# Optimization experiments

Measured on AMD Instinct MI355X. Metric: run time of the kernel, lower is better.

The kernel has to match this reference:

```python
import jax, jax.numpy as jnp
import numpy as np

N_NODES = 110
C = 4096  # in_channels = hidden = out_channels


def setup_inputs() -> dict:
    key = jax.random.key(0)
    ks = jax.random.split(key, 8)
    x = jax.random.normal(ks[0], (N_NODES, C), dtype=jnp.float32)
    adj = jax.random.randint(ks[1], (N_NODES, N_NODES), 0, 2, dtype=jnp.int32)
    # torch.nn.Linear weights stored [out_features, in_features]
    W2 = jax.random.normal(ks[2], (C, C), dtype=jnp.float32) / np.sqrt(C)
    b2 = jax.random.normal(ks[3], (C,), dtype=jnp.float32) * 0.01
    W1 = jax.random.normal(ks[4], (2 * C, C), dtype=jnp.float32) / np.sqrt(2 * C)
    b1 = jax.random.normal(ks[5], (C,), dtype=jnp.float32) * 0.01
    Wl = jax.random.normal(ks[6], (N_NODES, N_NODES), dtype=jnp.float32) / np.sqrt(N_NODES)
    bl = jax.random.normal(ks[7], (N_NODES,), dtype=jnp.float32) * 0.01
    # note: W1 is stored [in=2C, out=C]; W2 [in=C, out=C]; Wl [in=110, out=110]
    return {"x": x, "adj": adj, "W2": W2, "b2": b2, "W1": W1, "b1": b1, "Wl": Wl, "bl": bl}


def reference(x, adj, W2, b2, W1, b1, Wl, bl):
    # FeatGraphConv: h = lin2(x)
    h = x @ W2 + b2  # [N, C]
    # edge_index.nonzero(): adjacency -> edge list (i=src, j=dst); mean-aggregate
    # h[src] at dst. Dense equivalent: column-normalized mask matmul.
    mask = (adj != 0).astype(x.dtype)  # [N, N]
    deg = mask.sum(axis=0)  # in-degree of each target node j
    aggr = (mask.T @ h) / jnp.maximum(deg, 1.0)[:, None]  # [N, C]; 0 for isolated nodes (PyG mean)
    # update: lin1(cat(h, aggr)) then relu (in RegGNN.forward)
    out = jax.nn.relu(jnp.concatenate([h, aggr], axis=1) @ W1 + b1)  # [N, C]
    # x.t(); lin(110,110); x.t()
    out = (out.T @ Wl.T + bl).T  # [N, C]
    return out
```

## Files before the change

kernel.cpp:

```cpp
#include <hip/hip_runtime.h>
#include <hip/hip_fp16.h>

#define C 4096
#define NN 110
#define MPAD 112
#define BN 256
#define BK 32
#define ASTR 40

typedef _Float16 f16x8 __attribute__((ext_vector_type(8)));
typedef _Float16 f16x4 __attribute__((ext_vector_type(4)));
typedef float fx4 __attribute__((ext_vector_type(4)));

#define AS_GLB __attribute__((address_space(1)))
#define AS_LDS __attribute__((address_space(3)))

__global__ void prep1_kernel(const float* __restrict__ x, _Float16* __restrict__ A1) {
    int idx = blockIdx.x * 256 + threadIdx.x;
    int n = idx >> 12;
    float v = (n < NN) ? x[idx] : 0.f;
    A1[idx] = (_Float16)v;
}

__global__ __launch_bounds__(256, 2)
void mm_kernel(const _Float16* __restrict__ A, const float* __restrict__ B,
               float* __restrict__ Cacc, int lda, int kch) {
    __shared__ float    Bs[BK * BN];
    __shared__ _Float16 As[MPAD * ASTR];

    const int t   = threadIdx.x;
    const int w   = t >> 6;
    const int L   = t & 63;
    const int l15 = L & 15;
    const int q   = L >> 4;
    const int n0  = blockIdx.x * BN;
    const int k0  = blockIdx.y * kch;

    fx4 acc[7][4];
    #pragma unroll
    for (int mt = 0; mt < 7; ++mt)
        #pragma unroll
        for (int nt = 0; nt < 4; ++nt)
            acc[mt][nt] = (fx4){0.f, 0.f, 0.f, 0.f};

    #pragma unroll 1
    for (int kc = 0; kc < kch; kc += BK) {
        #pragma unroll
        for (int j = 0; j < 8; ++j) {
            const int row = w * 8 + j;
            const float* g = B + (size_t)(k0 + kc + row) * C + n0 + L * 4;
            __builtin_amdgcn_global_load_lds((const AS_GLB void*)g,
                                             (AS_LDS void*)(Bs + row * BN), 16, 0, 0);
        }
        #pragma unroll
        for (int i = 0; i < 4; ++i) {
            int idx = t + i * 256;
            if (idx < MPAD * 8) {
                int row = idx >> 3;
                int c4  = (idx & 7) * 4;
                f16x4 v = *(const f16x4*)(A + (size_t)row * lda + k0 + kc + c4);
                *(f16x4*)(As + row * ASTR + c4) = v;
            }
        }
        __syncthreads();
        f16x8 bfrag[4];
        #pragma unroll
        for (int nt = 0; nt < 4; ++nt)
            #pragma unroll
            for (int j = 0; j < 8; ++j)
                bfrag[nt][j] = (_Float16)Bs[(q * 8 + j) * BN + w * 64 + nt * 16 + l15];
        #pragma unroll
        for (int mt = 0; mt < 7; ++mt) {
            f16x8 af = *(const f16x8*)(As + (mt * 16 + l15) * ASTR + q * 8);
            #pragma unroll
            for (int nt = 0; nt < 4; ++nt)
                acc[mt][nt] = __builtin_amdgcn_mfma_f32_16x16x32_f16(af, bfrag[nt],
                                                                     acc[mt][nt], 0, 0, 0);
        }
        __syncthreads();
    }

    #pragma unroll
    for (int mt = 0; mt < 7; ++mt) {
        #pragma unroll
        for (int nt = 0; nt < 4; ++nt) {
            const int col = n0 + w * 64 + nt * 16 + l15;
            #pragma unroll
            for (int r = 0; r < 4; ++r) {
                int row = mt * 16 + q * 4 + r;
                if (row < NN)
                    atomicAdd(&Cacc[(size_t)row * C + col], acc[mt][nt][r]);
            }
        }
    }
}

__global__ __launch_bounds__(256)
void agg_kernel(const float* __restrict__ h_raw, const int* __restrict__ adj,
                const float* __restrict__ b2, _Float16* __restrict__ A3) {
    __shared__ float hb[NN * 16];
    __shared__ unsigned long long mlo[NN], mhi[NN];
    __shared__ float degs[NN];
    const int t  = threadIdx.x;
    const int c0 = blockIdx.x * 16;

    for (int idx = t; idx < NN * 16; idx += 256) {
        int n = idx >> 4, c = idx & 15;
        float v = h_raw[(size_t)n * C + c0 + c] + b2[c0 + c];
        hb[idx] = v;
        A3[(size_t)n * (2 * C) + c0 + c] = (_Float16)v;
    }
    if (t < 64) {
        int n  = NN + (t >> 5);
        int hs = (t >> 4) & 1;
        int c  = t & 15;
        A3[(size_t)n * (2 * C) + hs * C + c0 + c] = (_Float16)0.f;
    }
    if (t < NN) {
        int j = t;
        unsigned long long lo = 0, hi = 0;
        int dg = 0;
        for (int i = 0; i < 64; ++i) {
            int m = (adj[i * NN + j] != 0);
            lo |= ((unsigned long long)m) << i; dg += m;
        }
        for (int i = 64; i < NN; ++i) {
            int m = (adj[i * NN + j] != 0);
            hi |= ((unsigned long long)m) << (i - 64); dg += m;
        }
        mlo[j] = lo; mhi[j] = hi;
        degs[j] = (float)(dg > 0 ? dg : 1);
    }
    __syncthreads();
    for (int idx = t; idx < NN * 16; idx += 256) {
        int j = idx >> 4, c = idx & 15;
        unsigned long long lo = mlo[j], hi = mhi[j];
        float a = 0.f;
        #pragma unroll 2
        for (int i = 0; i < 64; ++i)
            a = fmaf((float)((lo >> i) & 1ull), hb[i * 16 + c], a);
        #pragma unroll 2
        for (int i = 64; i < NN; ++i)
            a = fmaf((float)((hi >> (i - 64)) & 1ull), hb[i * 16 + c], a);
        A3[(size_t)j * (2 * C) + C + c0 + c] = (_Float16)(a / degs[j]);
    }
}

__global__ __launch_bounds__(256)
void fin_kernel(const float* __restrict__ z_raw, const float* __restrict__ b1,
                const float* __restrict__ Wl, const float* __restrict__ bl,
                float* __restrict__ out) {
    __shared__ float zs[NN * 64];
    const int t  = threadIdx.x;
    const int c0 = blockIdx.x * 64;
    const int j  = blockIdx.y * 4 + (t >> 6);
    const int c  = t & 63;

    for (int idx = t; idx < NN * 64; idx += 256) {
        int k = idx >> 6, cc = idx & 63;
        float v = z_raw[(size_t)k * C + c0 + cc] + b1[c0 + cc];
        zs[idx] = fmaxf(v, 0.f);
    }
    __syncthreads();
    if (j < NN) {
        float a = bl[j];
        #pragma unroll 2
        for (int k = 0; k < NN; ++k)
            a += Wl[j * NN + k] * zs[k * 64 + c];
        out[(size_t)j * C + c0 + c] = a;
    }
}

extern "C" void kernel_launch(void* const* d_in, const int* in_sizes, int n_in,
                              void* d_out, int out_size, void* d_ws, size_t ws_size,
                              hipStream_t stream) {
    const float* x   = (const float*)d_in[0];
    const int*   adj = (const int*)d_in[1];
    const float* W2  = (const float*)d_in[2];
    const float* b2  = (const float*)d_in[3];
    const float* W1  = (const float*)d_in[4];
    const float* b1  = (const float*)d_in[5];
    const float* Wl  = (const float*)d_in[6];
    const float* bl  = (const float*)d_in[7];
    float* out = (float*)d_out;

    char* ws = (char*)d_ws;
    float*    h_raw = (float*)(ws);
    float*    z_raw = (float*)(ws + 1802240);
    _Float16* A1    = (_Float16*)(ws + 3604480);
    _Float16* A3    = (_Float16*)(ws + 4521984);

    hipMemsetAsync(d_ws, 0, 3604480, stream);
    prep1_kernel<<<(MPAD * C) / 256, 256, 0, stream>>>(x, A1);
    mm_kernel<<<dim3(C / BN, 32), 256, 0, stream>>>(A1, W2, h_raw, C, 128);
    agg_kernel<<<C / 16, 256, 0, stream>>>(h_raw, adj, b2, A3);
    mm_kernel<<<dim3(C / BN, 32), 256, 0, stream>>>(A3, W1, z_raw, 2 * C, 256);
    fin_kernel<<<dim3(C / 64, 28), 256, 0, stream>>>(z_raw, b1, Wl, bl, out);
}
```

Baseline: 414.9 us.

## Repack weights to tiled fp16, double-buffer GEMM, replace atomics with split-K partial sums

Adds a repack kernel that converts the fp32 weights into fp16 tiles laid out for MFMA B fragments, so the GEMM loads them directly with no per-element conversion in LDS. The GEMM now double-buffers its LDS stages, uses narrower 128-column tiles, and writes split-K partials to a buffer instead of issuing atomicAdds. Separate reductions in agg and a new zred kernel sum those partials. The repack runs on every call, which adds extra weight read and write traffic.

```diff
diff --git a/kernel.cpp b/kernel.cpp
--- a/kernel.cpp
+++ b/kernel.cpp
@@ -4,9 +4,6 @@
 #define C 4096
 #define NN 110
 #define MPAD 112
-#define BN 256
-#define BK 32
-#define ASTR 40
 
 typedef _Float16 f16x8 __attribute__((ext_vector_type(8)));
 typedef _Float16 f16x4 __attribute__((ext_vector_type(4)));
@@ -14,6 +11,43 @@
 
 #define AS_GLB __attribute__((address_space(1)))
 #define AS_LDS __attribute__((address_space(3)))
+
+__global__ __launch_bounds__(256, 2)
+void repack_kernel(const float* __restrict__ W, _Float16* __restrict__ B16, int K) {
+    __shared__ _Float16 Ls[1024 * 36];
+    const int t  = threadIdx.x;
+    const int kt = blockIdx.x;
+    const int cs = blockIdx.y;
+    const int Kt = K >> 5;
+
+    const float* src = W + (size_t)(kt * 32) * C + cs * 1024;
+    #pragma unroll 4
+    for (int i = 0; i < 32; ++i) {
+        int idx = t + i * 256;
+        int r   = idx >> 8;
+        int c4  = (idx & 255) * 4;
+        fx4 v = *(const fx4*)(src + (size_t)r * C + c4);
+        #pragma unroll
+        for (int j = 0; j < 4; ++j)
+            Ls[(c4 + j) * 36 + r] = (_Float16)v[j];
+    }
+    __syncthreads();
+    #pragma unroll 4
+    for (int i = 0; i < 16; ++i) {
+        int o   = t + i * 256;
+        int kk8 = (o & 3) * 8;
+        int c   = (o >> 2) & 127;
+        int nt8 = o >> 9;
+        const _Float16* lp = Ls + (nt8 * 128 + c) * 36 + kk8;
+        f16x4 a = *(const f16x4*)(lp);
+        f16x4 b = *(const f16x4*)(lp + 4);
+        f16x8 vv;
+        vv[0]=a[0]; vv[1]=a[1]; vv[2]=a[2]; vv[3]=a[3];
+        vv[4]=b[0]; vv[5]=b[1]; vv[6]=b[2]; vv[7]=b[3];
+        _Float16* dst = B16 + (((size_t)(cs * 8 + nt8) * Kt + kt) * 128 + c) * 32 + kk8;
+        *(f16x8*)dst = vv;
+    }
+}
 
 __global__ void prep1_kernel(const float* __restrict__ x, _Float16* __restrict__ A1) {
     int idx = blockIdx.x * 256 + threadIdx.x;
@@ -23,92 +57,105 @@
 }
 
 __global__ __launch_bounds__(256, 2)
-void mm_kernel(const _Float16* __restrict__ A, const float* __restrict__ B,
-               float* __restrict__ Cacc, int lda, int kch) {
-    __shared__ float    Bs[BK * BN];
-    __shared__ _Float16 As[MPAD * ASTR];
-
+void mm_kernel(const _Float16* __restrict__ A, const _Float16* __restrict__ B16,
+               float* __restrict__ pc, int lda, int kch) {
+    __shared__ _Float16 Bs[2][32 * 128];
+    __shared__ _Float16 As[2][MPAD * 40];
     const int t   = threadIdx.x;
     const int w   = t >> 6;
     const int L   = t & 63;
     const int l15 = L & 15;
     const int q   = L >> 4;
-    const int n0  = blockIdx.x * BN;
-    const int k0  = blockIdx.y * kch;
-
-    fx4 acc[7][4];
-    #pragma unroll
-    for (int mt = 0; mt < 7; ++mt)
-        #pragma unroll
-        for (int nt = 0; nt < 4; ++nt)
-            acc[mt][nt] = (fx4){0.f, 0.f, 0.f, 0.f};
-
-    #pragma unroll 1
-    for (int kc = 0; kc < kch; kc += BK) {
-        #pragma unroll
-        for (int j = 0; j < 8; ++j) {
-            const int row = w * 8 + j;
-            const float* g = B + (size_t)(k0 + kc + row) * C + n0 + L * 4;
-            __builtin_amdgcn_global_load_lds((const AS_GLB void*)g,
-                                             (AS_LDS void*)(Bs + row * BN), 16, 0, 0);
-        }
+    const int nt  = blockIdx.x;
+    const int kc  = blockIdx.y;
+    const int Kt  = lda >> 5;
+    const int kt0 = (kc * kch) >> 5;
+    const int stages = kch >> 5;
+
+    const _Float16* Bbase = B16 + ((size_t)nt * Kt + kt0) * 4096;
+
+    auto stageB = [&](int buf, int s) {
+        const _Float16* g = Bbase + (size_t)s * 4096 + (2 * w) * 512 + L * 8;
+        _Float16* l = &Bs[buf][(2 * w) * 512];
+        __builtin_amdgcn_global_load_lds((const AS_GLB void*)g, (AS_LDS void*)l, 16, 0, 0);
+        __builtin_amdgcn_global_load_lds((const AS_GLB void*)(g + 512),
+                                         (AS_LDS void*)(l + 512), 16, 0, 0);
+    };
+    auto stageA = [&](int buf, int s) {
+        int k0 = kc * kch + s * 32;
         #pragma unroll
         for (int i = 0; i < 4; ++i) {
             int idx = t + i * 256;
             if (idx < MPAD * 8) {
-                int row = idx >> 3;
-                int c4  = (idx & 7) * 4;
-                f16x4 v = *(const f16x4*)(A + (size_t)row * lda + k0 + kc + c4);
-                *(f16x4*)(As + row * ASTR + c4) = v;
+                int row = idx >> 3, c4 = (idx & 7) * 4;
+                f16x4 v = *(const f16x4*)(A + (size_t)row * lda + k0 + c4);
+                *(f16x4*)(&As[buf][row * 40 + c4]) = v;
             }
         }
+    };
+
+    fx4 acc[7][2];
+    #pragma unroll
+    for (int mt = 0; mt < 7; ++mt)
+        #pragma unroll
+        for (int n2 = 0; n2 < 2; ++n2)
+            acc[mt][n2] = (fx4){0.f, 0.f, 0.f, 0.f};
+
+    stageB(0, 0); stageA(0, 0);
+    #pragma unroll 1
+    for (int s = 0; s < stages; ++s) {
+        int buf = s & 1;
         __syncthreads();
-        f16x8 bfrag[4];
-        #pragma unroll
-        for (int nt = 0; nt < 4; ++nt)
+        if (s + 1 < stages) { stageB(buf ^ 1, s + 1); stageA(buf ^ 1, s + 1); }
+        f16x8 bfrag[2];
+        #pragma unroll
+        for (int n2 = 0; n2 < 2; ++n2) {
+            int cc = w * 32 + n2 * 16 + l15;
+            bfrag[n2] = *(const f16x8*)(&Bs[buf][cc * 32 + q * 8]);
+        }
+        #pragma unroll
+        for (int mt = 0; mt < 7; ++mt) {
+            f16x8 af = *(const f16x8*)(&As[buf][(mt * 16 + l15) * 40 + q * 8]);
             #pragma unroll
-            for (int j = 0; j < 8; ++j)
-                bfrag[nt][j] = (_Float16)Bs[(q * 8 + j) * BN + w * 64 + nt * 16 + l15];
-        #pragma unroll
-        for (int mt = 0; mt < 7; ++mt) {
-            f16x8 af = *(const f16x8*)(As + (mt * 16 + l15) * ASTR + q * 8);
-            #pragma unroll
-            for (int nt = 0; nt < 4; ++nt)
-                acc[mt][nt] = __builtin_amdgcn_mfma_f32_16x16x32_f16(af, bfrag[nt],
-                                                                     acc[mt][nt], 0, 0, 0);
-        }
-        __syncthreads();
-    }
-
+            for (int n2 = 0; n2 < 2; ++n2)
+                acc[mt][n2] = __builtin_amdgcn_mfma_f32_16x16x32_f16(af, bfrag[n2],
+                                                                     acc[mt][n2], 0, 0, 0);
+        }
+    }
+
+    float* base = pc + (size_t)(kc * 32 + nt) * NN * 128;
     #pragma unroll
-    for (int mt = 0; mt < 7; ++mt) {
-        #pragma unroll
-        for (int nt = 0; nt < 4; ++nt) {
-            const int col = n0 + w * 64 + nt * 16 + l15;
+    for (int mt = 0; mt < 7; ++mt)
+        #pragma unroll
+        for (int n2 = 0; n2 < 2; ++n2) {
+            int col = w * 32 + n2 * 16 + l15;
             #pragma unroll
             for (int r = 0; r < 4; ++r) {
                 int row = mt * 16 + q * 4 + r;
-                if (row < NN)
-                    atomicAdd(&Cacc[(size_t)row * C + col], acc[mt][nt][r]);
+                if (row < NN) base[(size_t)row * 128 + col] = acc[mt][n2][r];
             }
         }
-    }
 }
 
 __global__ __launch_bounds__(256)
-void agg_kernel(const float* __restrict__ h_raw, const int* __restrict__ adj,
+void agg_kernel(const float* __restrict__ pc1, const int* __restrict__ adj,
                 const float* __restrict__ b2, _Float16* __restrict__ A3) {
     __shared__ float hb[NN * 16];
     __shared__ unsigned long long mlo[NN], mhi[NN];
     __shared__ float degs[NN];
     const int t  = threadIdx.x;
     const int c0 = blockIdx.x * 16;
+    const int nt = c0 >> 7;
 
     for (int idx = t; idx < NN * 16; idx += 256) {
         int n = idx >> 4, c = idx & 15;
-        float v = h_raw[(size_t)n * C + c0 + c] + b2[c0 + c];
+        int cg = c0 + c, cl = cg & 127;
+        float v = b2[cg];
+        #pragma unroll 4
+        for (int kc = 0; kc < 16; ++kc)
+            v += pc1[((size_t)(kc * 32 + nt) * NN + n) * 128 + cl];
         hb[idx] = v;
-        A3[(size_t)n * (2 * C) + c0 + c] = (_Float16)v;
+        A3[(size_t)n * (2 * C) + cg] = (_Float16)v;
     }
     if (t < 64) {
         int n  = NN + (t >> 5);
@@ -147,9 +194,22 @@
 }
 
 __global__ __launch_bounds__(256)
-void fin_kernel(const float* __restrict__ z_raw, const float* __restrict__ b1,
-                const float* __restrict__ Wl, const float* __restrict__ bl,
-                float* __restrict__ out) {
+void zred_kernel(const float* __restrict__ pc2, const float* __restrict__ b1,
+                 float* __restrict__ z) {
+    int idx = blockIdx.x * 256 + threadIdx.x;
+    int n = idx >> 12;
+    int c = idx & 4095;
+    int nt = c >> 7, cl = c & 127;
+    float v = b1[c];
+    #pragma unroll 4
+    for (int kc = 0; kc < 16; ++kc)
+        v += pc2[((size_t)(kc * 32 + nt) * NN + n) * 128 + cl];
+    z[idx] = fmaxf(v, 0.f);
+}
+
+__global__ __launch_bounds__(256)
+void fin_kernel(const float* __restrict__ z, const float* __restrict__ Wl,
+                const float* __restrict__ bl, float* __restrict__ out) {
     __shared__ float zs[NN * 64];
     const int t  = threadIdx.x;
     const int c0 = blockIdx.x * 64;
@@ -158,8 +218,7 @@
 
     for (int idx = t; idx < NN * 64; idx += 256) {
         int k = idx >> 6, cc = idx & 63;
-        float v = z_raw[(size_t)k * C + c0 + cc] + b1[c0 + cc];
-        zs[idx] = fmaxf(v, 0.f);
+        zs[idx] = z[(size_t)k * C + c0 + cc];
     }
     __syncthreads();
     if (j < NN) {
@@ -185,15 +244,20 @@
     float* out = (float*)d_out;
 
     char* ws = (char*)d_ws;
-    float*    h_raw = (float*)(ws);
-    float*    z_raw = (float*)(ws + 1802240);
-    _Float16* A1    = (_Float16*)(ws + 3604480);
-    _Float16* A3    = (_Float16*)(ws + 4521984);
-
-    hipMemsetAsync(d_ws, 0, 3604480, stream);
+    _Float16* B16a = (_Float16*)(ws);
+    _Float16* B16b = (_Float16*)(ws + 33554432);
+    float*    pc1  = (float*)(ws + 100663296);
+    float*    pc2  = (float*)(ws + 129499136);
+    float*    z    = (float*)(ws + 158334976);
+    _Float16* A1   = (_Float16*)(ws + 160137216);
+    _Float16* A3   = (_Float16*)(ws + 161054720);
+
+    repack_kernel<<<dim3(128, 4), 256, 0, stream>>>(W2, B16a, 4096);
+    repack_kernel<<<dim3(256, 4), 256, 0, stream>>>(W1, B16b, 8192);
     prep1_kernel<<<(MPAD * C) / 256, 256, 0, stream>>>(x, A1);
-    mm_kernel<<<dim3(C / BN, 32), 256, 0, stream>>>(A1, W2, h_raw, C, 128);
-    agg_kernel<<<C / 16, 256, 0, stream>>>(h_raw, adj, b2, A3);
-    mm_kernel<<<dim3(C / BN, 32), 256, 0, stream>>>(A3, W1, z_raw, 2 * C, 256);
-    fin_kernel<<<dim3(C / 64, 28), 256, 0, stream>>>(z_raw, b1, Wl, bl, out);
-}
+    mm_kernel<<<dim3(32, 16), 256, 0, stream>>>(A1, B16a, pc1, 4096, 256);
+    agg_kernel<<<C / 16, 256, 0, stream>>>(pc1, adj, b2, A3);
+    mm_kernel<<<dim3(32, 16), 256, 0, stream>>>(A3, B16b, pc2, 8192, 512);
+    zred_kernel<<<(NN * C) / 256, 256, 0, stream>>>(pc2, b1, z);
+    fin_kernel<<<dim3(C / 64, 28), 256, 0, stream>>>(z, Wl, bl, out);
+}
```

New measurement: 396.4 us. -4.5%, faster.
